# Optimization experiments

Hardware: AMD Instinct MI355X
Metric: run time of the kernel (lower is better)

## Reference

```python
import jax, jax.numpy as jnp
import numpy as np

HP = 64  # padded height (next pow2 of 56)
WP = 64  # padded width
H, W = 56, 56


def fwht(x):
    """Walsh-Hadamard transform along last axis (n must be power of 2)."""
    n = x.shape[-1]
    h = 1
    while h < n:
        xr = x.reshape(*x.shape[:-1], n // (2 * h), 2 * h)
        a = xr[..., :h]
        b = xr[..., h:]
        x = jnp.concatenate([a + b, a - b], axis=-1).reshape(*x.shape[:-1], n)
        h *= 2
    return x


def fwht_axis(x, axis):
    if axis == -1:
        return fwht(x)
    return jnp.swapaxes(fwht(jnp.swapaxes(x, -1, axis)), -1, axis)


def ifwht_axis(x, axis):
    n = x.shape[axis]
    return fwht_axis(x, axis) / n


def setup_inputs() -> dict:
    key = jax.random.key(0)
    k1, k2, k3, k4 = jax.random.split(key, 4)
    x = jax.random.normal(k1, (64, 128, H, W), dtype=jnp.float32)
    # per-pod 1x1 conv weights (pods, out_ch, in_ch), kaiming-ish scale
    conv_w = jax.random.normal(k2, (2, 128, 128), dtype=jnp.float32) / np.sqrt(128.0)
    v = jax.random.uniform(k3, (2, HP, WP), dtype=jnp.float32)
    T = jax.random.uniform(k4, (2, HP, WP), dtype=jnp.float32) / 10.0
    return {"x": x, "conv_w": conv_w, "v": v, "T": T}


def reference(x, conv_w, v, T):
    # pad spatial dims to power of 2 (pad right/bottom)
    f0 = jnp.pad(x, ((0, 0), (0, 0), (0, HP - H), (0, WP - W)))
    # 2D WHT
    f1 = fwht_axis(f0, -1)
    f2 = fwht_axis(f1, -2)
    # per-pod: elementwise gate v, 1x1 conv, soft-threshold; then sum over pods
    # f3: (P, B, Cin, HP, WP)
    f3 = v[:, None, None, :, :] * f2[None]
    f4 = jnp.einsum('pbihw,poi->pbohw', f3, conv_w)
    thr = jax.nn.relu(T)[:, None, None, :, :]
    f5 = jnp.sign(f4) * jax.nn.relu(jnp.abs(f4) - thr)
    f6 = f5.sum(axis=0)
    # inverse 2D WHT
    f7 = ifwht_axis(f6, -1)
    f8 = ifwht_axis(f7, -2)
    y = f8[..., :H, :W]
    return y + x  # residual
```

## Files before the change

### kernel.cpp

```cpp
#include <hip/hip_runtime.h>

typedef unsigned short u16;
typedef unsigned int u32;
typedef __attribute__((ext_vector_type(8))) __bf16 bf16x8;
typedef __attribute__((ext_vector_type(8))) unsigned short u16x8;
typedef __attribute__((ext_vector_type(2))) unsigned int u32x2;
typedef __attribute__((ext_vector_type(4))) float f32x4;

__device__ __forceinline__ u16 f2bf(float f) {
  u32 u = __builtin_bit_cast(u32, f);
  u += 0x7FFFu + ((u >> 16) & 1u);
  return (u16)(u >> 16);
}
__device__ __forceinline__ float bf2f(u16 h) {
  u32 u = ((u32)h) << 16;
  return __builtin_bit_cast(float, u);
}

template <int M>
__device__ __forceinline__ void bfly16(float r[16]) {
#pragma unroll
  for (int j = 0; j < 16; ++j)
    if ((j & M) == 0) {
      float a = r[j], b = r[j | M];
      r[j] = a + b;
      r[j | M] = a - b;
    }
}

__global__ __launch_bounds__(256) void k0_wcat(const float* __restrict__ cw,
                                               u16* __restrict__ wc) {
  int i = blockIdx.x * 256 + threadIdx.x;
  wc[i] = f2bf(cw[i]);
}

__global__ __launch_bounds__(256) void k1_fwht(const float* __restrict__ x,
                                               u16* __restrict__ f2) {
  __shared__ float lds[64 * 68];
  const int t = threadIdx.x;
  const int b = blockIdx.x >> 4;
  const int cg = blockIdx.x & 15;
  const int hA = t >> 2, wq = t & 3;
  const int hg = t >> 4, rB = t & 15;
  const int wC = t & 63, rr = t >> 6;
  const bool hok = hA < 56;
  u16x8 outv[16];

#pragma unroll
  for (int pp = 0; pp < 8; ++pp) {
    const float* xp = x + (size_t)(b * 128 + cg * 8 + pp) * 3136;
    float r[16];
#pragma unroll
    for (int c4 = 0; c4 < 4; ++c4) {
      const int w0 = wq * 16 + c4 * 4;
      if (hok && w0 < 56) {
        const float4 v4 = *(const float4*)(xp + hA * 56 + w0);
        r[c4 * 4 + 0] = v4.x; r[c4 * 4 + 1] = v4.y;
        r[c4 * 4 + 2] = v4.z; r[c4 * 4 + 3] = v4.w;
      } else {
        r[c4 * 4 + 0] = 0.f; r[c4 * 4 + 1] = 0.f;
        r[c4 * 4 + 2] = 0.f; r[c4 * 4 + 3] = 0.f;
      }
    }
    bfly16<1>(r); bfly16<2>(r); bfly16<4>(r); bfly16<8>(r);
    if (pp) __syncthreads();
#pragma unroll
    for (int c4 = 0; c4 < 4; ++c4)
      *(float4*)&lds[hA * 68 + wq * 16 + c4 * 4] =
          make_float4(r[c4 * 4 + 0], r[c4 * 4 + 1], r[c4 * 4 + 2], r[c4 * 4 + 3]);
    __syncthreads();
    float q[16];
#pragma unroll
    for (int k = 0; k < 4; ++k)
#pragma unroll
      for (int d = 0; d < 4; ++d)
        q[k * 4 + d] = lds[(hg * 4 + d) * 68 + k * 16 + rB];
    bfly16<4>(q); bfly16<8>(q); bfly16<1>(q); bfly16<2>(q);
#pragma unroll
    for (int k = 0; k < 4; ++k)
#pragma unroll
      for (int d = 0; d < 4; ++d)
        lds[(hg * 4 + d) * 68 + k * 16 + rB] = q[k * 4 + d];
    __syncthreads();
    float s[16];
#pragma unroll
    for (int j = 0; j < 16; ++j) s[j] = lds[(4 * j + rr) * 68 + wC];
    bfly16<1>(s); bfly16<2>(s); bfly16<4>(s); bfly16<8>(s);
#pragma unroll
    for (int j = 0; j < 16; ++j) outv[j][pp] = f2bf(s[j]);
  }
  u16* dst = f2 + ((size_t)(b * 16 + cg) << 15);
#pragma unroll
  for (int j = 0; j < 16; ++j) {
    const int pos = (4 * j + rr) * 64 + wC;
    *(u16x8*)(dst + (size_t)pos * 8) = outv[j];
  }
}

__global__ __launch_bounds__(256) void k2_mix(u16* __restrict__ fg,
                                              const u16* __restrict__ wc,
                                              const float* __restrict__ vv,
                                              const float* __restrict__ tt) {
  const int t = threadIdx.x;
  const int b = blockIdx.x >> 6;
  const int p0 = (blockIdx.x & 63) << 6;
  u16* fb = fg + ((size_t)b << 19);
  const int wv = t >> 6, l = t & 63, lr = l & 15, lq = l >> 4;
  f32x4 acc[2][2][4] = {};
#pragma unroll
  for (int q = 0; q < 4; ++q) {
    bf16x8 af[2][2];
#pragma unroll
    for (int fp = 0; fp < 2; ++fp)
#pragma unroll
      for (int fm = 0; fm < 2; ++fm) {
        const int row = fp * 128 + wv * 32 + fm * 16 + lr;
        af[fp][fm] = __builtin_bit_cast(
            bf16x8, *(const u16x8*)(wc + row * 128 + 32 * q + 8 * lq));
      }
#pragma unroll
    for (int fn = 0; fn < 4; ++fn) {
      const bf16x8 bq = __builtin_bit_cast(
          bf16x8, *(const u16x8*)(fb + (size_t)(4 * q + lq) * 32768 +
                                  (size_t)(p0 + fn * 16 + lr) * 8));
#pragma unroll
      for (int fp = 0; fp < 2; ++fp)
#pragma unroll
        for (int fm = 0; fm < 2; ++fm)
          acc[fp][fm][fn] = __builtin_amdgcn_mfma_f32_16x16x32_bf16(
              af[fp][fm], bq, acc[fp][fm][fn], 0, 0, 0);
    }
  }
  __syncthreads();
#pragma unroll
  for (int fn = 0; fn < 4; ++fn) {
    const int pos = p0 + fn * 16 + lr;
    const float v0 = vv[pos], v1 = vv[4096 + pos];
    const float t0 = fmaxf(tt[pos], 0.f), t1 = fmaxf(tt[4096 + pos], 0.f);
#pragma unroll
    for (int fm = 0; fm < 2; ++fm) {
      u16 w[4];
#pragma unroll
      for (int rg = 0; rg < 4; ++rg) {
        const float z0 = v0 * acc[0][fm][fn][rg];
        const float z1 = v1 * acc[1][fm][fn][rg];
        const float s0v = copysignf(fmaxf(fabsf(z0) - t0, 0.f), z0);
        const float s1v = copysignf(fmaxf(fabsf(z1) - t1, 0.f), z1);
        w[rg] = f2bf(s0v + s1v);
      }
      const int og = wv * 4 + fm * 2 + (lq >> 1);
      u32x2 pk;
      pk[0] = (u32)w[0] | ((u32)w[1] << 16);
      pk[1] = (u32)w[2] | ((u32)w[3] << 16);
      *(u32x2*)(fb + (size_t)og * 32768 + (size_t)pos * 8 + (lq & 1) * 4) = pk;
    }
  }
}

__global__ __launch_bounds__(256) void k3_iwht(const u16* __restrict__ g,
                                               const float* __restrict__ x,
                                               float* __restrict__ y) {
  __shared__ float lds[64 * 68];
  const int t = threadIdx.x;
  const int b = blockIdx.x >> 4;
  const int og = blockIdx.x & 15;
  const u16* gb = g + ((size_t)(b * 16 + og) << 15);
  const int hA = t >> 2, wq = t & 3;
  const int hg = t >> 4, rB = t & 15;
  const int wC = t & 63, rr = t >> 6;
  u16x8 inv[16];
#pragma unroll
  for (int e = 0; e < 16; ++e)
    inv[e] = *(const u16x8*)(gb + (size_t)(hA * 64 + wq * 16 + e) * 8);

#pragma unroll
  for (int pp = 0; pp < 8; ++pp) {
    float r[16];
#pragma unroll
    for (int e = 0; e < 16; ++e) r[e] = bf2f(inv[e][pp]);
    bfly16<1>(r); bfly16<2>(r); bfly16<4>(r); bfly16<8>(r);
    if (pp) __syncthreads();
#pragma unroll
    for (int c4 = 0; c4 < 4; ++c4)
      *(float4*)&lds[hA * 68 + wq * 16 + c4 * 4] =
          make_float4(r[c4 * 4 + 0], r[c4 * 4 + 1], r[c4 * 4 + 2], r[c4 * 4 + 3]);
    __syncthreads();
    float q[16];
#pragma unroll
    for (int k = 0; k < 4; ++k)
#pragma unroll
      for (int d = 0; d < 4; ++d)
        q[k * 4 + d] = lds[(hg * 4 + d) * 68 + k * 16 + rB];
    bfly16<4>(q); bfly16<8>(q); bfly16<1>(q); bfly16<2>(q);
#pragma unroll
    for (int k = 0; k < 4; ++k)
#pragma unroll
      for (int d = 0; d < 4; ++d)
        lds[(hg * 4 + d) * 68 + k * 16 + rB] = q[k * 4 + d];
    __syncthreads();
    float s[16];
#pragma unroll
    for (int j = 0; j < 16; ++j) s[j] = lds[(4 * j + rr) * 68 + wC];
    bfly16<1>(s); bfly16<2>(s); bfly16<4>(s); bfly16<8>(s);
    if (wC < 56) {
      const size_t plane = (size_t)(b * 128 + og * 8 + pp) * 3136;
#pragma unroll
      for (int j = 0; j < 14; ++j) {
        const int h = 4 * j + rr;
        const size_t idx = plane + (size_t)(h * 56 + wC);
        y[idx] = x[idx] + s[j] * (1.f / 4096.f);
      }
    }
  }
}

extern "C" void kernel_launch(void* const* d_in, const int* in_sizes, int n_in,
                              void* d_out, int out_size, void* d_ws, size_t ws_size,
                              hipStream_t stream) {
  const float* x = (const float*)d_in[0];
  const float* cw = (const float*)d_in[1];
  const float* v = (const float*)d_in[2];
  const float* T = (const float*)d_in[3];
  float* y = (float*)d_out;

  u16* f2 = (u16*)d_ws;
  u16* wcat = (u16*)((char*)d_ws + 67108864);

  k0_wcat<<<128, 256, 0, stream>>>(cw, wcat);
  k1_fwht<<<1024, 256, 0, stream>>>(x, f2);
  k2_mix<<<4096, 256, 0, stream>>>(f2, wcat, v, T);
  k3_iwht<<<1024, 256, 0, stream>>>(f2, x, y);
}
```

Before: 140.3 us.

## Pre-swizzle conv weights into MFMA fragment order and hoist all k2 loads

The weight conversion kernel now writes bf16 weights already permuted into per-lane MFMA fragment order, so each lane in the mix kernel reads a contiguous 16-byte chunk instead of strided rows. The mix kernel issues all B-fragment, A-fragment and gate/threshold loads up front, before the MFMA loop, so memory latency overlaps, and it adds a launch-bounds occupancy hint. The cost is higher register pressure from holding all fragments live, which could limit occupancy or cause spills.

```diff
diff --git a/kernel.cpp b/kernel.cpp
--- a/kernel.cpp
+++ b/kernel.cpp
@@ -30,8 +30,17 @@
 
 __global__ __launch_bounds__(256) void k0_wcat(const float* __restrict__ cw,
                                                u16* __restrict__ wc) {
-  int i = blockIdx.x * 256 + threadIdx.x;
-  wc[i] = f2bf(cw[i]);
+  const int i = blockIdx.x * 256 + threadIdx.x;
+  const int j = i & 7;
+  const int lr = (i >> 3) & 15;
+  const int lq = (i >> 7) & 3;
+  const int q = (i >> 9) & 3;
+  const int fm = (i >> 11) & 1;
+  const int wv = (i >> 12) & 3;
+  const int fp = (i >> 14) & 1;
+  const int row = fp * 128 + wv * 32 + fm * 16 + lr;
+  const int k = q * 32 + lq * 8 + j;
+  wc[i] = f2bf(cw[row * 128 + k]);
 }
 
 __global__ __launch_bounds__(256) void k1_fwht(const float* __restrict__ x,
@@ -97,62 +106,77 @@
   }
 }
 
-__global__ __launch_bounds__(256) void k2_mix(u16* __restrict__ fg,
-                                              const u16* __restrict__ wc,
-                                              const float* __restrict__ vv,
-                                              const float* __restrict__ tt) {
+__global__ __launch_bounds__(256, 2) void k2_mix(u16* __restrict__ fg,
+                                                 const u16* __restrict__ wc,
+                                                 const float* __restrict__ vv,
+                                                 const float* __restrict__ tt) {
   const int t = threadIdx.x;
   const int b = blockIdx.x >> 6;
   const int p0 = (blockIdx.x & 63) << 6;
   u16* fb = fg + ((size_t)b << 19);
   const int wv = t >> 6, l = t & 63, lr = l & 15, lq = l >> 4;
+
+  bf16x8 bfr[4][4];
+#pragma unroll
+  for (int q = 0; q < 4; ++q)
+#pragma unroll
+    for (int fn = 0; fn < 4; ++fn)
+      bfr[q][fn] = __builtin_bit_cast(
+          bf16x8, *(const u16x8*)(fb + ((size_t)(4 * q + lq) << 15) +
+                                  (size_t)(p0 + fn * 16 + lr) * 8));
+  bf16x8 afr[4][2][2];
+#pragma unroll
+  for (int q = 0; q < 4; ++q)
+#pragma unroll
+    for (int fp = 0; fp < 2; ++fp)
+#pragma unroll
+      for (int fm = 0; fm < 2; ++fm) {
+        const int frag_id = ((fp * 4 + wv) * 2 + fm) * 4 + q;
+        afr[q][fp][fm] = __builtin_bit_cast(
+            bf16x8, *(const u16x8*)(wc + (frag_id << 9) + l * 8));
+      }
+  float v0s[4], v1s[4], t0s[4], t1s[4];
+#pragma unroll
+  for (int fn = 0; fn < 4; ++fn) {
+    const int pos = p0 + fn * 16 + lr;
+    v0s[fn] = vv[pos];
+    v1s[fn] = vv[4096 + pos];
+    t0s[fn] = fmaxf(tt[pos], 0.f);
+    t1s[fn] = fmaxf(tt[4096 + pos], 0.f);
+  }
+
   f32x4 acc[2][2][4] = {};
 #pragma unroll
-  for (int q = 0; q < 4; ++q) {
-    bf16x8 af[2][2];
-#pragma unroll
-    for (int fp = 0; fp < 2; ++fp)
-#pragma unroll
-      for (int fm = 0; fm < 2; ++fm) {
-        const int row = fp * 128 + wv * 32 + fm * 16 + lr;
-        af[fp][fm] = __builtin_bit_cast(
-            bf16x8, *(const u16x8*)(wc + row * 128 + 32 * q + 8 * lq));
-      }
-#pragma unroll
-    for (int fn = 0; fn < 4; ++fn) {
-      const bf16x8 bq = __builtin_bit_cast(
-          bf16x8, *(const u16x8*)(fb + (size_t)(4 * q + lq) * 32768 +
-                                  (size_t)(p0 + fn * 16 + lr) * 8));
+  for (int q = 0; q < 4; ++q)
+#pragma unroll
+    for (int fn = 0; fn < 4; ++fn)
 #pragma unroll
       for (int fp = 0; fp < 2; ++fp)
 #pragma unroll
         for (int fm = 0; fm < 2; ++fm)
           acc[fp][fm][fn] = __builtin_amdgcn_mfma_f32_16x16x32_bf16(
-              af[fp][fm], bq, acc[fp][fm][fn], 0, 0, 0);
-    }
-  }
+              afr[q][fp][fm], bfr[q][fn], acc[fp][fm][fn], 0, 0, 0);
+
   __syncthreads();
 #pragma unroll
   for (int fn = 0; fn < 4; ++fn) {
     const int pos = p0 + fn * 16 + lr;
-    const float v0 = vv[pos], v1 = vv[4096 + pos];
-    const float t0 = fmaxf(tt[pos], 0.f), t1 = fmaxf(tt[4096 + pos], 0.f);
 #pragma unroll
     for (int fm = 0; fm < 2; ++fm) {
       u16 w[4];
 #pragma unroll
       for (int rg = 0; rg < 4; ++rg) {
-        const float z0 = v0 * acc[0][fm][fn][rg];
-        const float z1 = v1 * acc[1][fm][fn][rg];
-        const float s0v = copysignf(fmaxf(fabsf(z0) - t0, 0.f), z0);
-        const float s1v = copysignf(fmaxf(fabsf(z1) - t1, 0.f), z1);
+        const float z0 = v0s[fn] * acc[0][fm][fn][rg];
+        const float z1 = v1s[fn] * acc[1][fm][fn][rg];
+        const float s0v = copysignf(fmaxf(fabsf(z0) - t0s[fn], 0.f), z0);
+        const float s1v = copysignf(fmaxf(fabsf(z1) - t1s[fn], 0.f), z1);
         w[rg] = f2bf(s0v + s1v);
       }
       const int og = wv * 4 + fm * 2 + (lq >> 1);
       u32x2 pk;
       pk[0] = (u32)w[0] | ((u32)w[1] << 16);
       pk[1] = (u32)w[2] | ((u32)w[3] << 16);
-      *(u32x2*)(fb + (size_t)og * 32768 + (size_t)pos * 8 + (lq & 1) * 4) = pk;
+      *(u32x2*)(fb + ((size_t)og << 15) + (size_t)pos * 8 + (lq & 1) * 4) = pk;
     }
   }
 }
```

Measured after the change: 124.6 us. -11.2%, faster.
